# Performance work log

Hardware: AMD Instinct MI355X
Metric: run time of the kernel (lower is better)

The kernel has to match this reference:

```python
import jax, jax.numpy as jnp
import numpy as np

B, N, D, FUSE, A = 512, 1024, 1024, 1024, 256


def setup_inputs() -> dict:
    key = jax.random.key(0)
    ks = jax.random.split(key, 6)
    return {
        "confounder_set": jax.random.normal(ks[0], (N, D), dtype=jnp.float32),
        "fuse_rep": jax.random.normal(ks[1], (B, FUSE), dtype=jnp.float32),
        "probabilities": jax.random.uniform(ks[2], (1, N), dtype=jnp.float32),
        "Wq": jax.random.normal(ks[3], (FUSE, A), dtype=jnp.float32) / np.sqrt(FUSE),
        "Wk": jax.random.normal(ks[4], (D, A), dtype=jnp.float32) / np.sqrt(D),
        "wt": jax.random.normal(ks[5], (A,), dtype=jnp.float32) / np.sqrt(A),
    }


def reference(confounder_set, fuse_rep, probabilities, Wq, Wk, wt):
    # query: [B, A], key: [N, A]
    q = fuse_rep @ Wq
    k = confounder_set @ Wk
    # broadcasted add + tanh -> [B, N, A]
    fuse = jnp.tanh(q[:, None, :] + k[None, :, :])
    # scoring linear -> [B, N]
    scores = jnp.einsum("bna,a->bn", fuse, wt)
    attn = jax.nn.softmax(scores, axis=1)           # [B, N]
    probs = probabilities[0]                        # [N]  (transpose(0,1) of [1,N])
    # probability-weighted confounder sum -> [B, D]
    fin = jnp.einsum("bn,nd->bd", attn * probs[None, :], confounder_set)
    return fin
```

## Files before the change

kernel.cpp:

```cpp
#include <hip/hip_runtime.h>
#include <hip/hip_bf16.h>

#define B 512
#define N 1024
#define D 1024
#define FUSE 1024
#define A 256

typedef float f32x4 __attribute__((ext_vector_type(4)));
typedef short bf16x8 __attribute__((ext_vector_type(8)));
typedef unsigned short u16x4 __attribute__((ext_vector_type(4)));

__device__ __forceinline__ float fast_exp2(float x) { return __builtin_amdgcn_exp2f(x); }
__device__ __forceinline__ float fast_rcp(float x)  { return __builtin_amdgcn_rcpf(x); }

static constexpr float TANH_C = 2.8853900817779268f;
static constexpr float LOG2E  = 1.4426950408889634f;

__device__ __forceinline__ unsigned short f2bf(float x) {
    __hip_bfloat16 h = __float2bfloat16(x);
    return *reinterpret_cast<unsigned short*>(&h);
}

__global__ __launch_bounds__(256) void cast_kernel(
    const float* __restrict__ fuse, const float* __restrict__ conf,
    const float* __restrict__ Wq, const float* __restrict__ Wk,
    short* __restrict__ fuse_bf, short* __restrict__ conf_bf,
    short* __restrict__ confT, short* __restrict__ WqT, short* __restrict__ WkT)
{
    __shared__ float tile[64 * 65];
    int bid = blockIdx.x;
    const float* src; short* dstS = nullptr; short* dstT = nullptr;
    int r0, c0, spitch; float scale = 1.0f;
    if (bid < 128) {
        src = fuse; dstS = fuse_bf; spitch = FUSE;
        r0 = (bid >> 4) * 64; c0 = (bid & 15) * 64;
    } else if (bid < 384) {
        int b = bid - 128; src = conf; dstS = conf_bf; dstT = confT; spitch = D;
        r0 = (b >> 4) * 64; c0 = (b & 15) * 64;
    } else if (bid < 448) {
        int b = bid - 384; src = Wq; dstT = WqT; spitch = A; scale = TANH_C;
        r0 = (b >> 2) * 64; c0 = (b & 3) * 64;
    } else {
        int b = bid - 448; src = Wk; dstT = WkT; spitch = A; scale = TANH_C;
        r0 = (b >> 2) * 64; c0 = (b & 3) * 64;
    }
    const int tr = threadIdx.x >> 4, tc = (threadIdx.x & 15) * 4;

    f32x4 v[4];
#pragma unroll
    for (int i = 0; i < 4; ++i) {
        v[i] = *(const f32x4*)(src + (size_t)(r0 + tr + 16 * i) * spitch + c0 + tc);
#pragma unroll
        for (int j = 0; j < 4; ++j) v[i][j] *= scale;
    }
    if (dstS) {
#pragma unroll
        for (int i = 0; i < 4; ++i) {
            u16x4 o;
#pragma unroll
            for (int j = 0; j < 4; ++j) o[j] = f2bf(v[i][j]);
            *(u16x4*)(dstS + (size_t)(r0 + tr + 16 * i) * spitch + c0 + tc) = o;
        }
    }
    if (dstT) {
#pragma unroll
        for (int i = 0; i < 4; ++i)
#pragma unroll
            for (int j = 0; j < 4; ++j) tile[(tr + 16 * i) * 65 + tc + j] = v[i][j];
        __syncthreads();
#pragma unroll
        for (int i = 0; i < 4; ++i) {
            int orow = tr + 16 * i;
            u16x4 o;
#pragma unroll
            for (int j = 0; j < 4; ++j) o[j] = f2bf(tile[(tc + j) * 65 + orow]);
            *(u16x4*)(dstT + (size_t)(c0 + orow) * 1024 + r0 + tc) = o;
        }
    }
}

__device__ __forceinline__ void gemm64(
    const short* __restrict__ Ag, const short* __restrict__ Btg,
    float* __restrict__ C, int K, int ldc, int m0, int n0,
    short* As, short* Bs)
{
    const int tid = threadIdx.x;
    const int wid = tid >> 6, lane = tid & 63;
    const int wm = wid >> 1, wn = wid & 1;
    const int lr = lane & 15;
    const int lk = (lane >> 4) * 8;
    const int cr = (lane >> 4) * 4;

    f32x4 acc[2][2] = {};

    for (int k0 = 0; k0 < K; k0 += 64) {
#pragma unroll
        for (int p = 0; p < 2; ++p) {
            int idx = tid + p * 256;
            int row = idx >> 3, c8 = idx & 7;
            bf16x8 va = *(const bf16x8*)(Ag  + (size_t)(m0 + row) * K + k0 + c8 * 8);
            bf16x8 vb = *(const bf16x8*)(Btg + (size_t)(n0 + row) * K + k0 + c8 * 8);
            int off = (row * 64 + c8 * 8) ^ ((row & 7) << 3);
            *(bf16x8*)(As + off) = va;
            *(bf16x8*)(Bs + off) = vb;
        }
        __syncthreads();
        bf16x8 af[2][2], bf[2][2];
#pragma unroll
        for (int ks = 0; ks < 2; ++ks)
#pragma unroll
            for (int i = 0; i < 2; ++i) {
                int r = wm * 32 + i * 16 + lr;
                af[i][ks] = *(const bf16x8*)(As + ((r * 64 + ks * 32 + lk) ^ ((r & 7) << 3)));
                int c = wn * 32 + i * 16 + lr;
                bf[i][ks] = *(const bf16x8*)(Bs + ((c * 64 + ks * 32 + lk) ^ ((c & 7) << 3)));
            }
#pragma unroll
        for (int ks = 0; ks < 2; ++ks)
#pragma unroll
            for (int am = 0; am < 2; ++am)
#pragma unroll
                for (int bn = 0; bn < 2; ++bn)
                    acc[am][bn] = __builtin_amdgcn_mfma_f32_16x16x32_bf16(
                        af[am][ks], bf[bn][ks], acc[am][bn], 0, 0, 0);
        __syncthreads();
    }
#pragma unroll
    for (int am = 0; am < 2; ++am)
#pragma unroll
        for (int bn = 0; bn < 2; ++bn) {
            float* cp = C + (size_t)(m0 + wm * 32 + am * 16 + cr) * ldc
                          + n0 + wn * 32 + bn * 16 + lr;
#pragma unroll
            for (int r = 0; r < 4; ++r) cp[(size_t)r * ldc] = acc[am][bn][r];
        }
}

__global__ __launch_bounds__(256) void qk_gemm_kernel(
    const short* __restrict__ fuse_bf, const short* __restrict__ conf_bf,
    const short* __restrict__ WqT, const short* __restrict__ WkT,
    float* __restrict__ qbuf, float* __restrict__ kbuf)
{
    __shared__ short As[64 * 64];
    __shared__ short Bs[64 * 64];
    int bid = blockIdx.x;
    if (bid < 32) {
        gemm64(fuse_bf, WqT, qbuf, FUSE, A, (bid >> 2) * 64, (bid & 3) * 64, As, Bs);
    } else {
        bid -= 32;
        gemm64(conf_bf, WkT, kbuf, D, A, (bid >> 2) * 64, (bid & 3) * 64, As, Bs);
    }
}

__global__ __launch_bounds__(256) void fin_gemm_kernel(
    const short* __restrict__ wb, const short* __restrict__ confT,
    float* __restrict__ out)
{
    __shared__ short As[64 * 64];
    __shared__ short Bs[64 * 64];
    gemm64(wb, confT, out, N, D, blockIdx.y * 64, blockIdx.x * 64, As, Bs);
}

__global__ __launch_bounds__(256) void scores_kernel(
    const float* __restrict__ qbuf, const float* __restrict__ kbuf,
    const float* __restrict__ wt, float* __restrict__ s)
{
    __shared__ f32x4 qs[32 * 64];
    __shared__ f32x4 ks[32 * 64];
    const int tid = threadIdx.x;
    const int b0 = blockIdx.x * 32;
    const int n0 = blockIdx.y * 32;

    const f32x4* q4 = (const f32x4*)qbuf + (size_t)b0 * 64;
    const f32x4* k4 = (const f32x4*)kbuf + (size_t)n0 * 64;
#pragma unroll
    for (int j = 0; j < 8; ++j) {
        int idx = tid + j * 256;
        int r = idx >> 6, c = idx & 63;
        qs[idx] = q4[idx];
        ks[r * 64 + (c ^ (r & 15))] = k4[idx];
    }
    __syncthreads();

    const int bl = tid >> 5;
    const int nl = tid & 31;
    const f32x4* wt4 = (const f32x4*)wt;

    float acc0 = 0.f, acc1 = 0.f, acc2 = 0.f, acc3 = 0.f;
    for (int a4 = 0; a4 < 64; ++a4) {
        f32x4 kv = ks[nl * 64 + (a4 ^ (nl & 15))];
        f32x4 wv = wt4[a4];
        f32x4 q0 = qs[(bl) * 64 + a4];
        f32x4 q1 = qs[(bl + 8) * 64 + a4];
        f32x4 q2 = qs[(bl + 16) * 64 + a4];
        f32x4 q3 = qs[(bl + 24) * 64 + a4];
#pragma unroll
        for (int c = 0; c < 4; ++c) {
            float kc = kv[c], wc = wv[c];
            acc0 += wc * fast_rcp(fast_exp2(q0[c] + kc) + 1.0f);
            acc1 += wc * fast_rcp(fast_exp2(q1[c] + kc) + 1.0f);
            acc2 += wc * fast_rcp(fast_exp2(q2[c] + kc) + 1.0f);
            acc3 += wc * fast_rcp(fast_exp2(q3[c] + kc) + 1.0f);
        }
    }
    s[(size_t)(b0 + bl) * N + n0 + nl]      = -2.0f * acc0;
    s[(size_t)(b0 + bl + 8) * N + n0 + nl]  = -2.0f * acc1;
    s[(size_t)(b0 + bl + 16) * N + n0 + nl] = -2.0f * acc2;
    s[(size_t)(b0 + bl + 24) * N + n0 + nl] = -2.0f * acc3;
}

__global__ __launch_bounds__(256) void softmax_kernel(
    const float* __restrict__ s, const float* __restrict__ probs,
    short* __restrict__ wbuf)
{
    const int b = blockIdx.x, tid = threadIdx.x;
    const f32x4* s4 = (const f32x4*)(s + (size_t)b * N);
    f32x4 v = s4[tid];

    float m = fmaxf(fmaxf(v[0], v[1]), fmaxf(v[2], v[3]));
    for (int off = 32; off > 0; off >>= 1) m = fmaxf(m, __shfl_xor(m, off));
    __shared__ float redm[4];
    __shared__ float reds[4];
    const int wid = tid >> 6, lane = tid & 63;
    if (lane == 0) redm[wid] = m;
    __syncthreads();
    m = fmaxf(fmaxf(redm[0], redm[1]), fmaxf(redm[2], redm[3]));

    f32x4 e;
#pragma unroll
    for (int c = 0; c < 4; ++c) e[c] = fast_exp2((v[c] - m) * LOG2E);
    float sum = e[0] + e[1] + e[2] + e[3];
    for (int off = 32; off > 0; off >>= 1) sum += __shfl_xor(sum, off);
    if (lane == 0) reds[wid] = sum;
    __syncthreads();
    sum = reds[0] + reds[1] + reds[2] + reds[3];

    const float inv = fast_rcp(sum);
    const f32x4* p4 = (const f32x4*)probs;
    f32x4 p = p4[tid];
    u16x4 o;
#pragma unroll
    for (int c = 0; c < 4; ++c) o[c] = f2bf(e[c] * inv * p[c]);
    ((u16x4*)(wbuf + (size_t)b * N))[tid] = o;
}

extern "C" void kernel_launch(void* const* d_in, const int* in_sizes, int n_in,
                              void* d_out, int out_size, void* d_ws, size_t ws_size,
                              hipStream_t stream) {
    const float* conf     = (const float*)d_in[0];
    const float* fuse_rep = (const float*)d_in[1];
    const float* probs    = (const float*)d_in[2];
    const float* Wq       = (const float*)d_in[3];
    const float* Wk       = (const float*)d_in[4];
    const float* wt       = (const float*)d_in[5];
    float* out = (float*)d_out;

    char* w = (char*)d_ws;
    float* qbuf   = (float*)(w);
    float* kbuf   = (float*)(w + 524288);
    float* sbuf   = (float*)(w + 1572864);
    short* fuse_bf= (short*)(w + 3670016);
    short* conf_bf= (short*)(w + 4718592);
    short* confT  = (short*)(w + 6815744);
    short* WqT    = (short*)(w + 8912896);
    short* WkT    = (short*)(w + 9437184);
    short* wbuf   = (short*)(w);

    hipLaunchKernelGGL(cast_kernel, dim3(512), dim3(256), 0, stream,
                       fuse_rep, conf, Wq, Wk, fuse_bf, conf_bf, confT, WqT, WkT);
    hipLaunchKernelGGL(qk_gemm_kernel, dim3(96), dim3(256), 0, stream,
                       fuse_bf, conf_bf, WqT, WkT, qbuf, kbuf);
    hipLaunchKernelGGL(scores_kernel, dim3(B / 32, N / 32), dim3(256), 0, stream,
                       qbuf, kbuf, wt, sbuf);
    hipLaunchKernelGGL(softmax_kernel, dim3(B), dim3(256), 0, stream,
                       sbuf, probs, wbuf);
    hipLaunchKernelGGL(fin_gemm_kernel, dim3(D / 64, B / 64), dim3(256), 0, stream,
                       wbuf, confT, out);
}
```

Before: 123.5 us.

## Double-buffer GEMM tiles with direct global-to-LDS async loads

Replaces the register-staged global→LDS copy in the shared 64x64 bf16 GEMM with __builtin_amdgcn_global_load_lds into a double-buffered LDS tile. The next K-tile is prefetched while MFMAs run on the current one. The XOR swizzle is moved to the source address so the async writes still land in bank-conflict-free order. This aims to hide global load latency and cut the per-iteration register round-trip, at the cost of doubled LDS per block and a vmcnt(0) wait plus barrier each iteration.

```diff
diff --git a/kernel.cpp b/kernel.cpp
--- a/kernel.cpp
+++ b/kernel.cpp
@@ -80,41 +80,61 @@
     }
 }
 
-__device__ __forceinline__ void gemm64(
+__device__ __forceinline__ void gemm64_pipe(
     const short* __restrict__ Ag, const short* __restrict__ Btg,
     float* __restrict__ C, int K, int ldc, int m0, int n0,
-    short* As, short* Bs)
+    char* As, char* Bs)
 {
     const int tid = threadIdx.x;
-    const int wid = tid >> 6, lane = tid & 63;
-    const int wm = wid >> 1, wn = wid & 1;
-    const int lr = lane & 15;
-    const int lk = (lane >> 4) * 8;
-    const int cr = (lane >> 4) * 4;
+    const int w = tid >> 6, l = tid & 63;
+    const int wm = w >> 1, wn = w & 1;
+    const int lr = l & 15;
+    const int cr = (l >> 4) * 4;
+    const int rsub = l >> 3;
+    const int ssrc = ((l & 7) ^ rsub) << 3;
+
+    auto stage = [&](int buf, int k0) {
+#pragma unroll
+        for (int p = 0; p < 2; ++p) {
+            int chunk = (w << 1) | p;
+            int row = (chunk << 3) | rsub;
+            int ldsoff = (buf << 13) | (chunk << 10);
+            __builtin_amdgcn_global_load_lds(
+                (const __attribute__((address_space(1))) unsigned int*)
+                    (Ag + (size_t)(m0 + row) * K + k0 + ssrc),
+                (__attribute__((address_space(3))) unsigned int*)(As + ldsoff),
+                16, 0, 0);
+            __builtin_amdgcn_global_load_lds(
+                (const __attribute__((address_space(1))) unsigned int*)
+                    (Btg + (size_t)(n0 + row) * K + k0 + ssrc),
+                (__attribute__((address_space(3))) unsigned int*)(Bs + ldsoff),
+                16, 0, 0);
+        }
+    };
 
     f32x4 acc[2][2] = {};
-
-    for (int k0 = 0; k0 < K; k0 += 64) {
-#pragma unroll
-        for (int p = 0; p < 2; ++p) {
-            int idx = tid + p * 256;
-            int row = idx >> 3, c8 = idx & 7;
-            bf16x8 va = *(const bf16x8*)(Ag  + (size_t)(m0 + row) * K + k0 + c8 * 8);
-            bf16x8 vb = *(const bf16x8*)(Btg + (size_t)(n0 + row) * K + k0 + c8 * 8);
-            int off = (row * 64 + c8 * 8) ^ ((row & 7) << 3);
-            *(bf16x8*)(As + off) = va;
-            *(bf16x8*)(Bs + off) = vb;
-        }
-        __syncthreads();
-        bf16x8 af[2][2], bf[2][2];
+    const int nt = K >> 6;
+
+    stage(0, 0);
+    asm volatile("s_waitcnt vmcnt(0)" ::: "memory");
+    __builtin_amdgcn_s_barrier();
+
+    int cur = 0;
+    for (int t = 0; t < nt; ++t) {
+        if (t + 1 < nt) stage(cur ^ 1, (t + 1) << 6);
+
+        const char* Ab = As + (cur << 13);
+        const char* Bb = Bs + (cur << 13);
+        bf16x8 af[2][2], bq[2][2];
 #pragma unroll
         for (int ks = 0; ks < 2; ++ks)
 #pragma unroll
             for (int i = 0; i < 2; ++i) {
+                int j = ks * 64 + ((l >> 4) << 4);
                 int r = wm * 32 + i * 16 + lr;
-                af[i][ks] = *(const bf16x8*)(As + ((r * 64 + ks * 32 + lk) ^ ((r & 7) << 3)));
+                af[i][ks] = *(const bf16x8*)(Ab + r * 128 + (j ^ ((r & 7) << 4)));
                 int c = wn * 32 + i * 16 + lr;
-                bf[i][ks] = *(const bf16x8*)(Bs + ((c * 64 + ks * 32 + lk) ^ ((c & 7) << 3)));
+                bq[i][ks] = *(const bf16x8*)(Bb + c * 128 + (j ^ ((c & 7) << 4)));
             }
 #pragma unroll
         for (int ks = 0; ks < 2; ++ks)
@@ -123,9 +143,13 @@
 #pragma unroll
                 for (int bn = 0; bn < 2; ++bn)
                     acc[am][bn] = __builtin_amdgcn_mfma_f32_16x16x32_bf16(
-                        af[am][ks], bf[bn][ks], acc[am][bn], 0, 0, 0);
-        __syncthreads();
-    }
+                        af[am][ks], bq[bn][ks], acc[am][bn], 0, 0, 0);
+
+        asm volatile("s_waitcnt vmcnt(0)" ::: "memory");
+        __builtin_amdgcn_s_barrier();
+        cur ^= 1;
+    }
+
 #pragma unroll
     for (int am = 0; am < 2; ++am)
 #pragma unroll
@@ -142,14 +166,14 @@
     const short* __restrict__ WqT, const short* __restrict__ WkT,
     float* __restrict__ qbuf, float* __restrict__ kbuf)
 {
-    __shared__ short As[64 * 64];
-    __shared__ short Bs[64 * 64];
+    __shared__ char As[16384];
+    __shared__ char Bs[16384];
     int bid = blockIdx.x;
     if (bid < 32) {
-        gemm64(fuse_bf, WqT, qbuf, FUSE, A, (bid >> 2) * 64, (bid & 3) * 64, As, Bs);
+        gemm64_pipe(fuse_bf, WqT, qbuf, FUSE, A, (bid >> 2) * 64, (bid & 3) * 64, As, Bs);
     } else {
         bid -= 32;
-        gemm64(conf_bf, WkT, kbuf, D, A, (bid >> 2) * 64, (bid & 3) * 64, As, Bs);
+        gemm64_pipe(conf_bf, WkT, kbuf, D, A, (bid >> 2) * 64, (bid & 3) * 64, As, Bs);
     }
 }
 
@@ -157,9 +181,9 @@
     const short* __restrict__ wb, const short* __restrict__ confT,
     float* __restrict__ out)
 {
-    __shared__ short As[64 * 64];
-    __shared__ short Bs[64 * 64];
-    gemm64(wb, confT, out, N, D, blockIdx.y * 64, blockIdx.x * 64, As, Bs);
+    __shared__ char As[16384];
+    __shared__ char Bs[16384];
+    gemm64_pipe(wb, confT, out, N, D, blockIdx.y * 64, blockIdx.x * 64, As, Bs);
 }
 
 __global__ __launch_bounds__(256) void scores_kernel(
```

Result: slower. 129.5 us (+4.9%).
